# Optimization experiments

Hardware: AMD Instinct MI355X
Metric: run time of the kernel (lower is better)

Reference implementation:

```python
import jax, jax.numpy as jnp
import numpy as np

B, N = 16, 16384
K = 16        # num_keypoints
LATENT = 128
CAGE = 8
BN_EPS = 1e-5


def setup_inputs():
    key = jax.random.key(0)
    ks = jax.random.split(key, 40)
    def rn(i, shape, s=1.0):
        return jax.random.normal(ks[i], shape, dtype=jnp.float32) * s
    inp = {
        "source_points": rn(0, (B, N, 3)),
        "target_points": rn(1, (B, N, 3)),
        "enc_w1": rn(2, (64, 3), 0.3), "enc_b1": rn(3, (64,), 0.1),
        "bn1_gamma": 1.0 + rn(4, (64,), 0.1), "bn1_beta": rn(5, (64,), 0.1),
        "bn1_mean": rn(6, (64,), 0.1), "bn1_var": 0.5 + jax.random.uniform(ks[7], (64,), dtype=jnp.float32),
        "enc_w2": rn(8, (128, 64), 0.1), "enc_b2": rn(9, (128,), 0.1),
        "bn2_gamma": 1.0 + rn(10, (128,), 0.1), "bn2_beta": rn(11, (128,), 0.1),
        "bn2_mean": rn(12, (128,), 0.1), "bn2_var": 0.5 + jax.random.uniform(ks[13], (128,), dtype=jnp.float32),
        "enc_w3": rn(14, (LATENT, 128), 0.1), "enc_b3": rn(15, (LATENT,), 0.1),
        "bn3_gamma": 1.0 + rn(16, (LATENT,), 0.1), "bn3_beta": rn(17, (LATENT,), 0.1),
        "bn3_mean": rn(18, (LATENT,), 0.1), "bn3_var": 0.5 + jax.random.uniform(ks[19], (LATENT,), dtype=jnp.float32),
        "kp_w1": rn(20, (128, LATENT), 0.1), "kp_b1": rn(21, (128,), 0.1),
        "kp_w2": rn(22, (K * 3, 128), 0.1), "kp_b2": rn(23, (K * 3,), 0.1),
        "cg_w1": rn(24, (128, K * 3), 0.1), "cg_b1": rn(25, (128,), 0.1),
        "cg_w2": rn(26, (CAGE ** 3 * 3, 128), 0.05), "cg_b2": rn(27, (CAGE ** 3 * 3,), 0.01),
    }
    return inp


def _bn(x, g, b, m, v):
    # inference-mode BatchNorm1d over channel (last) dim
    return (x - m) * jax.lax.rsqrt(v + BN_EPS) * g + b


def _encode(pts, w1, b1, g1, be1, m1, v1, w2, b2, g2, be2, m2, v2, w3, b3, g3, be3, m3, v3):
    # pointwise 1x1 convs == per-point linear layers; pts: (B, N, 3)
    h = jax.nn.relu(_bn(jnp.einsum('bnc,oc->bno', pts, w1) + b1, g1, be1, m1, v1))
    h = jax.nn.relu(_bn(jnp.einsum('bnc,oc->bno', h, w2) + b2, g2, be2, m2, v2))
    h = jax.nn.relu(_bn(jnp.einsum('bnc,oc->bno', h, w3) + b3, g3, be3, m3, v3))
    return h.max(axis=1)  # global max-pool -> (B, LATENT)


def _fps_one(pts, kps):
    # pts: (N,3), kps: (K,3). Same math as the torch loop: iterative farthest-point
    # selection; recomputing cdist to selected[:i] each step == incremental min-dist.
    # squared distances preserve argmax/min of euclidean distances.
    d0 = jnp.sum((pts[:, None, :] - kps[None, :, :]) ** 2, -1).min(axis=1)
    sel0 = pts[jnp.argmax(d0)]
    mind = jnp.sum((pts - sel0) ** 2, -1)
    def step(mind, _):
        sel = pts[jnp.argmax(mind)]
        return jnp.minimum(mind, jnp.sum((pts - sel) ** 2, -1)), sel
    _, sels = jax.lax.scan(step, mind, None, length=K - 1)
    return jnp.concatenate([sel0[None], sels], axis=0)  # (K, 3)


def _fps(points, keypoints):
    return jax.vmap(_fps_one)(points, keypoints)


def _cage_deform(pts, disp):
    # pts: (B,N,3), disp: (B,C,C,C,3). Batched trilinear interpolation on the cage.
    C = CAGE
    lin = jnp.linspace(0.0, 1.0, C)
    grid = jnp.stack(jnp.meshgrid(lin, lin, lin, indexing='ij'), axis=-1)
    cage = grid[None] + disp
    cf = cage.reshape(cage.shape[0], C * C * C, 3)
    pmin = pts.min(axis=1, keepdims=True)
    pmax = pts.max(axis=1, keepdims=True)
    t = (pts - pmin) / (pmax - pmin + 1e-6) * (C - 1)
    idx = jnp.clip(t.astype(jnp.int32), 0, C - 2)   # trunc == floor (t >= 0)
    w = t - idx.astype(t.dtype)
    u, v, z = idx[..., 0], idx[..., 1], idx[..., 2]
    wx, wy, wz = w[..., 0:1], w[..., 1:2], w[..., 2:3]
    def corner(du, dv, dz):
        flat = (u + du) * C * C + (v + dv) * C + (z + dz)      # (B,N)
        flat = jnp.broadcast_to(flat[..., None], flat.shape + (3,))
        return jnp.take_along_axis(cf, flat, axis=1)            # (B,N,3)
    d = ((1 - wx) * (1 - wy) * (1 - wz) * corner(0, 0, 0)
         + wx * (1 - wy) * (1 - wz) * corner(1, 0, 0)
         + (1 - wx) * wy * (1 - wz) * corner(0, 1, 0)
         + wx * wy * (1 - wz) * corner(1, 1, 0)
         + (1 - wx) * (1 - wy) * wz * corner(0, 0, 1)
         + wx * (1 - wy) * wz * corner(1, 0, 1)
         + (1 - wx) * wy * wz * corner(0, 1, 1)
         + wx * wy * wz * corner(1, 1, 1))
    return pts + d


def reference(source_points, target_points, enc_w1, enc_b1, bn1_gamma, bn1_beta, bn1_mean, bn1_var, enc_w2, enc_b2, bn2_gamma, bn2_beta, bn2_mean, bn2_var, enc_w3, enc_b3, bn3_gamma, bn3_beta, bn3_mean, bn3_var, kp_w1, kp_b1, kp_w2, kp_b2, cg_w1, cg_b1, cg_w2, cg_b2):
    enc = lambda p: _encode(p, enc_w1, enc_b1, bn1_gamma, bn1_beta, bn1_mean, bn1_var,
                            enc_w2, enc_b2, bn2_gamma, bn2_beta, bn2_mean, bn2_var,
                            enc_w3, enc_b3, bn3_gamma, bn3_beta, bn3_mean, bn3_var)
    src_lat = enc(source_points)
    tgt_lat = enc(target_points)
    kp = lambda lat: (jax.nn.relu(lat @ kp_w1.T + kp_b1) @ kp_w2.T + kp_b2).reshape(-1, K, 3)
    src_kp = _fps(source_points, kp(src_lat))
    tgt_kp = _fps(target_points, kp(tgt_lat))
    diff = (tgt_kp - src_kp).reshape(-1, K * 3)
    disp = (jax.nn.relu(diff @ cg_w1.T + cg_b1) @ cg_w2.T + cg_b2).reshape(-1, CAGE, CAGE, CAGE, 3)
    deformed = _cage_deform(source_points, disp)
    return (deformed, src_kp, tgt_kp)
```

## Files before the change

kernel.cpp:

```cpp
#include <hip/hip_runtime.h>

#define B_ 16
#define N_ 16384
#define K_ 16

enum : int {
  WS_LAT  = 0,
  WS_SEL  = 5632,
  WS_PMIN = 7168,
  WS_PMAX = 7216,
  WS_CF   = 7264,
  WS_W1F  = 31840,
  WS_B1F  = 32032,
  WS_WB2H = 32096,
  WS_WB2L = 36192,
  WS_B2F  = 40288,
  WS_WB3H = 40416,
  WS_B3F  = 56800,
  WS_WB3L = 56928,
  WS_END  = 73312
};

enum : int { OUT_DEF=0, OUT_SRCKP=786432, OUT_TGTKP=787200 };

typedef _Float16 f16x8 __attribute__((ext_vector_type(8)));
typedef _Float16 f16x2 __attribute__((ext_vector_type(2)));
typedef float    f32x4 __attribute__((ext_vector_type(4)));

__device__ __forceinline__ float dist2rn(float px,float py,float pz,float sx,float sy,float sz){
  float dx=__fsub_rn(px,sx), dy=__fsub_rn(py,sy), dz=__fsub_rn(pz,sz);
  return __fadd_rn(__fadd_rn(__fmul_rn(dx,dx),__fmul_rn(dy,dy)),__fmul_rn(dz,dz));
}

struct EncW {
  const float *w1,*b1,*g1,*be1,*m1,*v1;
  const float *w2,*b2,*g2,*be2,*m2,*v2;
  const float *w3,*b3,*g3,*be3,*m3,*v3;
};

__device__ __forceinline__ float bn_scale(const float* g, const float* v, int ch){
  return g[ch] * (1.0f / sqrtf(v[ch] + 1e-5f));
}

__global__ void prep_kernel(EncW a, float* ws){
  const int stride = gridDim.x*blockDim.x;
  const int tid = blockIdx.x*blockDim.x + threadIdx.x;
  for (int i=tid;i<4096;i+=stride)
    ws[WS_LAT+i] = 0.0f;
  for (int i=tid;i<192;i+=stride){
    int o=i/3;
    ws[WS_W1F+i] = a.w1[i] * bn_scale(a.g1,a.v1,o);
  }
  for (int i=tid;i<64;i+=stride){
    float s = bn_scale(a.g1,a.v1,i);
    ws[WS_B1F+i] = (a.b1[i] - a.m1[i])*s + a.be1[i];
  }
  for (int i=tid;i<8192;i+=stride){
    int j = i & 7, frag = i >> 3;
    int l = frag & 63, nk = frag >> 6;
    int kt = nk & 1, nt = nk >> 1;
    int c = kt*32 + ((l>>4)<<3) + j;
    int o = nt*16 + (l&15);
    float v = a.w2[o*64+c] * bn_scale(a.g2,a.v2,o);
    _Float16 h = (_Float16)v;
    ((_Float16*)(ws+WS_WB2H))[i] = h;
    ((_Float16*)(ws+WS_WB2L))[i] = (_Float16)(v - (float)h);
  }
  for (int i=tid;i<128;i+=stride){
    float s = bn_scale(a.g2,a.v2,i);
    ws[WS_B2F+i] = (a.b2[i] - a.m2[i])*s + a.be2[i];
  }
  for (int i=tid;i<32768;i+=stride){
    int j = i & 7, frag = i >> 3;
    int l = frag & 63, nk = frag >> 6;
    int kt = nk & 3, nt = nk >> 2;
    int c = kt*32 + ((l>>4)<<3) + j;
    int o = nt*16 + (l&15);
    float v = a.w3[o*128+c] * bn_scale(a.g3,a.v3,o);
    _Float16 h = (_Float16)v;
    ((_Float16*)(ws+WS_WB3H))[i] = h;
    ((_Float16*)(ws+WS_WB3L))[i] = (_Float16)(v - (float)h);
  }
  for (int i=tid;i<128;i+=stride){
    float s = bn_scale(a.g3,a.v3,i);
    ws[WS_B3F+i] = (a.b3[i] - a.m3[i])*s + a.be3[i];
  }
}

__global__ __launch_bounds__(256, 4) void encode_kernel(const float* __restrict__ src,
                                                        const float* __restrict__ tgt,
                                                        const float* __restrict__ ws,
                                                        float* __restrict__ lat){
  const int cloud = blockIdx.y;
  const int tile  = blockIdx.x;
  const int t = threadIdx.x;
  const int lane = t & 63;
  const int wn = __builtin_amdgcn_readfirstlane(t >> 6);
  const int lr = lane & 15;
  const int lg = lane >> 4;

  __shared__ alignas(16) _Float16 A[16384];
  _Float16* AH1 = A;
  _Float16* AL1 = A + 4096;
  _Float16* AH2 = A;
  _Float16* AL2 = A + 8192;

  const float* base = ((cloud < B_) ? (src + (size_t)cloud*N_*3)
                                    : (tgt + (size_t)(cloud-B_)*N_*3))
                      + (size_t)tile*64*3;

  {
    const int pt = t >> 2, q = t & 3;
    const float x = base[pt*3+0], y = base[pt*3+1], z = base[pt*3+2];
    const float* w1 = ws + WS_W1F;
    const float* b1 = ws + WS_B1F;
    const int swz = (pt & 7) << 3;
    #pragma unroll
    for (int cc = 0; cc < 16; cc += 2){
      const int o = q*16 + cc;
      float v0 = fmaf(w1[o*3+2], z, fmaf(w1[o*3+1], y, w1[o*3+0]*x)) + b1[o];
      float v1 = fmaf(w1[o*3+5], z, fmaf(w1[o*3+4], y, w1[o*3+3]*x)) + b1[o+1];
      v0 = fmaxf(v0, 0.0f); v1 = fmaxf(v1, 0.0f);
      f16x2 h, l;
      h[0] = (_Float16)v0;              h[1] = (_Float16)v1;
      l[0] = (_Float16)(v0 - (float)h[0]); l[1] = (_Float16)(v1 - (float)h[1]);
      const int idx = (pt*64 + o) ^ swz;
      *(f16x2*)&AH1[idx] = h;
      *(f16x2*)&AL1[idx] = l;
    }
  }
  __syncthreads();

  f32x4 acc2[4][2];
  #pragma unroll
  for (int m=0;m<4;m++){
    #pragma unroll
    for (int n=0;n<2;n++) acc2[m][n] = (f32x4){0.f,0.f,0.f,0.f};
  }
  {
    const _Float16* wb2h = (const _Float16*)(ws + WS_WB2H);
    const _Float16* wb2l = (const _Float16*)(ws + WS_WB2L);
    const int swz = (lr & 7) << 3;
    #pragma unroll
    for (int kt=0; kt<2; kt++){
      f16x8 bh[2], bl[2];
      #pragma unroll
      for (int n=0;n<2;n++){
        const int fi = (((wn*2+n)*2 + kt)*64 + lane)*8;
        bh[n] = *(const f16x8*)(wb2h + fi);
        bl[n] = *(const f16x8*)(wb2l + fi);
      }
      #pragma unroll
      for (int m=0;m<4;m++){
        const int row = m*16 + lr;
        const int idx = (row*64 + kt*32 + lg*8) ^ swz;
        const f16x8 ah = *(const f16x8*)&AH1[idx];
        const f16x8 al = *(const f16x8*)&AL1[idx];
        #pragma unroll
        for (int n=0;n<2;n++){
          acc2[m][n] = __builtin_amdgcn_mfma_f32_16x16x32_f16(ah, bh[n], acc2[m][n], 0,0,0);
          acc2[m][n] = __builtin_amdgcn_mfma_f32_16x16x32_f16(ah, bl[n], acc2[m][n], 0,0,0);
          acc2[m][n] = __builtin_amdgcn_mfma_f32_16x16x32_f16(al, bh[n], acc2[m][n], 0,0,0);
        }
      }
    }
  }
  __syncthreads();

  {
    const float* b2 = ws + WS_B2F;
    #pragma unroll
    for (int n=0;n<2;n++){
      const int ch = wn*32 + n*16 + lr;
      const float b = b2[ch];
      #pragma unroll
      for (int m=0;m<4;m++){
        #pragma unroll
        for (int r=0;r<4;r++){
          const int row = m*16 + lg*4 + r;
          const float v = fmaxf(acc2[m][n][r] + b, 0.0f);
          const _Float16 hi = (_Float16)v;
          const _Float16 lo = (_Float16)(v - (float)hi);
          const int idx = (row*128 + ch) ^ ((row & 7) << 3);
          AH2[idx] = hi;
          AL2[idx] = lo;
        }
      }
    }
  }
  __syncthreads();

  f32x4 acc3[4][2];
  #pragma unroll
  for (int m=0;m<4;m++){
    #pragma unroll
    for (int n=0;n<2;n++) acc3[m][n] = (f32x4){0.f,0.f,0.f,0.f};
  }
  {
    const _Float16* wb3h = (const _Float16*)(ws + WS_WB3H);
    const _Float16* wb3l = (const _Float16*)(ws + WS_WB3L);
    const int swz = (lr & 7) << 3;
    #pragma unroll
    for (int kt=0; kt<4; kt++){
      f16x8 bh[2], bl[2];
      #pragma unroll
      for (int n=0;n<2;n++){
        const int fi = (((wn*2+n)*4 + kt)*64 + lane)*8;
        bh[n] = *(const f16x8*)(wb3h + fi);
        bl[n] = *(const f16x8*)(wb3l + fi);
      }
      #pragma unroll
      for (int m=0;m<4;m++){
        const int row = m*16 + lr;
        const int idx = (row*128 + kt*32 + lg*8) ^ swz;
        const f16x8 ah = *(const f16x8*)&AH2[idx];
        const f16x8 al = *(const f16x8*)&AL2[idx];
        #pragma unroll
        for (int n=0;n<2;n++){
          acc3[m][n] = __builtin_amdgcn_mfma_f32_16x16x32_f16(ah, bh[n], acc3[m][n], 0,0,0);
          acc3[m][n] = __builtin_amdgcn_mfma_f32_16x16x32_f16(ah, bl[n], acc3[m][n], 0,0,0);
          acc3[m][n] = __builtin_amdgcn_mfma_f32_16x16x32_f16(al, bh[n], acc3[m][n], 0,0,0);
        }
      }
    }
  }

  {
    const float* b3 = ws + WS_B3F;
    #pragma unroll
    for (int n=0;n<2;n++){
      const int ch = wn*32 + n*16 + lr;
      const float b = b3[ch];
      float x = 0.0f;
      #pragma unroll
      for (int m=0;m<4;m++){
        #pragma unroll
        for (int r=0;r<4;r++)
          x = fmaxf(x, acc3[m][n][r] + b);
      }
      x = fmaxf(x, __shfl_xor(x, 16, 64));
      x = fmaxf(x, __shfl_xor(x, 32, 64));
      if (lane < 16)
        atomicMax((unsigned*)(lat + cloud*128 + ch), __float_as_uint(x));
    }
  }
}

__device__ __forceinline__ void fps_round(int r, int t, int wv,
                                          float bv, int bi, float bx, float by, float bz,
                                          float (*cv)[16], int (*ci)[16],
                                          float (*cx)[16], float (*cy)[16], float (*cz)[16],
                                          float* ws, float* out, int cloud,
                                          float& s0, float& s1, float& s2){
  float v = bv; int i = bi;
  #pragma unroll
  for (int m=1;m<64;m<<=1){
    float v2=__shfl_xor(v,m,64); int i2=__shfl_xor(i,m,64);
    if (v2 > v || (v2 == v && i2 < i)){ v=v2; i=i2; }
  }
  const int p = r & 1;
  if ((i >> 4) == t){ cv[p][wv]=v; ci[p][wv]=i; cx[p][wv]=bx; cy[p][wv]=by; cz[p][wv]=bz; }
  __syncthreads();
  float wvv = cv[p][0]; int wi = ci[p][0]; int slot = 0;
  #pragma unroll
  for (int e=1;e<16;e++){
    float v2=cv[p][e]; int i2=ci[p][e];
    if (v2 > wvv || (v2 == wvv && i2 < wi)){ wvv=v2; wi=i2; slot=e; }
  }
  s0 = cx[p][slot]; s1 = cy[p][slot]; s2 = cz[p][slot];
  if (t == 0){
    float* sw = ws + WS_SEL + cloud*48 + r*3;
    sw[0]=s0; sw[1]=s1; sw[2]=s2;
    size_t o = (cloud<B_) ? (size_t)(OUT_SRCKP + cloud*48 + r*3)
                          : (size_t)(OUT_TGTKP + (cloud-B_)*48 + r*3);
    out[o]=s0; out[o+1]=s1; out[o+2]=s2;
  }
}

__global__ __launch_bounds__(1024, 4) void fps_kernel(const float* __restrict__ src,
                                                      const float* __restrict__ tgt,
                                                      const float* __restrict__ kw1,
                                                      const float* __restrict__ kb1,
                                                      const float* __restrict__ kw2,
                                                      const float* __restrict__ kb2,
                                                      float* ws, float* out){
  const int cloud = blockIdx.x; const int t = threadIdx.x;
  const int wv = t >> 6;
  const int lane = t & 63;
  const float* base = (cloud < B_) ? (src + (size_t)cloud*N_*3)
                                   : (tgt + (size_t)cloud*N_*3 - (size_t)B_*N_*3);
  __shared__ float kpl[48];
  __shared__ float h[128];
  __shared__ float cv[2][16]; __shared__ int ci[2][16];
  __shared__ float cx[2][16]; __shared__ float cy[2][16]; __shared__ float cz[2][16];
  __shared__ float red[96];

  float px[16], py[16], pz[16];
  {
    const float4* b4 = (const float4*)(base + (size_t)t*48);
    #pragma unroll
    for (int q=0;q<4;q++){
      float4 va=b4[q*3], vb=b4[q*3+1], vc=b4[q*3+2];
      px[q*4  ]=va.x; py[q*4  ]=va.y; pz[q*4  ]=va.z;
      px[q*4+1]=va.w; py[q*4+1]=vb.x; pz[q*4+1]=vb.y;
      px[q*4+2]=vb.z; py[q*4+2]=vb.w; pz[q*4+2]=vc.x;
      px[q*4+3]=vc.y; py[q*4+3]=vc.z; pz[q*4+3]=vc.w;
    }
  }

  if (cloud < B_){
    float mn0=3.4e38f,mn1=3.4e38f,mn2=3.4e38f, mx0=-3.4e38f,mx1=-3.4e38f,mx2=-3.4e38f;
    #pragma unroll
    for (int k=0;k<16;k++){
      mn0=fminf(mn0,px[k]); mn1=fminf(mn1,py[k]); mn2=fminf(mn2,pz[k]);
      mx0=fmaxf(mx0,px[k]); mx1=fmaxf(mx1,py[k]); mx2=fmaxf(mx2,pz[k]);
    }
    #pragma unroll
    for (int m=1;m<64;m<<=1){
      mn0=fminf(mn0,__shfl_xor(mn0,m,64)); mx0=fmaxf(mx0,__shfl_xor(mx0,m,64));
      mn1=fminf(mn1,__shfl_xor(mn1,m,64)); mx1=fmaxf(mx1,__shfl_xor(mx1,m,64));
      mn2=fminf(mn2,__shfl_xor(mn2,m,64)); mx2=fmaxf(mx2,__shfl_xor(mx2,m,64));
    }
    if (lane==0){
      red[wv*6+0]=mn0; red[wv*6+1]=mn1; red[wv*6+2]=mn2;
      red[wv*6+3]=mx0; red[wv*6+4]=mx1; red[wv*6+5]=mx2;
    }
    __syncthreads();
    if (t < 6){
      float v = red[t];
      for (int e=1;e<16;e++){
        float v2 = red[e*6+t];
        v = (t<3) ? fminf(v,v2) : fmaxf(v,v2);
      }
      if (t<3) ws[WS_PMIN + cloud*3 + t] = v;
      else     ws[WS_PMAX + cloud*3 + (t-3)] = v;
    }
  }
  __syncthreads();

  const float* lat = ws + WS_LAT + cloud*128;
  if (t < 128){
    float acc = kb1[t];
    const float* w = kw1 + t*128;
    for (int c=0;c<128;c++) acc = fmaf(lat[c], w[c], acc);
    h[t] = fmaxf(acc, 0.0f);
  }
  __syncthreads();
  if (t < 48){
    float acc = kb2[t];
    const float* w = kw2 + t*128;
    for (int c=0;c<128;c++) acc = fmaf(h[c], w[c], acc);
    kpl[t] = acc;
  }
  __syncthreads();

  float mind[16];
  #pragma unroll
  for (int k=0;k<16;k++) mind[k] = 3.4028235e38f;
  for (int j=0;j<K_;j++){
    const float sx=kpl[j*3], sy=kpl[j*3+1], sz=kpl[j*3+2];
    #pragma unroll
    for (int k=0;k<16;k++)
      mind[k] = fminf(mind[k], dist2rn(px[k],py[k],pz[k], sx,sy,sz));
  }

  float bv = -1.0f; int bi = 0; float bx=0.f, by=0.f, bz=0.f;
  #pragma unroll
  for (int k=0;k<16;k++){
    if (mind[k] > bv){ bv=mind[k]; bi=t*16+k; bx=px[k]; by=py[k]; bz=pz[k]; }
  }
  float s0, s1, s2;
  fps_round(0, t, wv, bv, bi, bx, by, bz, cv, ci, cx, cy, cz, ws, out, cloud, s0, s1, s2);

  bv = -1.0f; bi = 0;
  #pragma unroll
  for (int k=0;k<16;k++){
    float d = dist2rn(px[k],py[k],pz[k], s0,s1,s2);
    mind[k] = d;
    if (d > bv){ bv=d; bi=t*16+k; bx=px[k]; by=py[k]; bz=pz[k]; }
  }
  fps_round(1, t, wv, bv, bi, bx, by, bz, cv, ci, cx, cy, cz, ws, out, cloud, s0, s1, s2);

  for (int r=2; r<K_; ++r){
    bv = -1.0f; bi = 0;
    #pragma unroll
    for (int k=0;k<16;k++){
      float d = dist2rn(px[k],py[k],pz[k], s0,s1,s2);
      float m = fminf(mind[k], d);
      mind[k] = m;
      if (m > bv){ bv=m; bi=t*16+k; bx=px[k]; by=py[k]; bz=pz[k]; }
    }
    fps_round(r, t, wv, bv, bi, bx, by, bz, cv, ci, cx, cy, cz, ws, out, cloud, s0, s1, s2);
  }
}

__global__ void cage_mlp_kernel(const float* __restrict__ ws,
                                const float* __restrict__ cw1, const float* __restrict__ cb1,
                                const float* __restrict__ cw2, const float* __restrict__ cb2,
                                float* __restrict__ wsm){
  const int b = blockIdx.x >> 2, part = blockIdx.x & 3;
  const int t = threadIdx.x;
  __shared__ float diff[48]; __shared__ float h[128];
  if (t<48) diff[t] = __fsub_rn(ws[WS_SEL + (B_+b)*48 + t], ws[WS_SEL + b*48 + t]);
  __syncthreads();
  if (t<128){
    const float* w = cw1 + t*48;
    float acc = cb1[t];
    for (int j=0;j<48;j++) acc = fmaf(diff[j], w[j], acc);
    h[t] = fmaxf(acc, 0.0f);
  }
  __syncthreads();
  for (int o = part*384 + t; o < part*384 + 384; o += 256){
    const float* w = cw2 + o*128;
    float acc = cb2[o];
    for (int c=0;c<128;c++) acc = fmaf(h[c], w[c], acc);
    int flat = o/3, coord = o - flat*3;
    int u = flat>>6, v=(flat>>3)&7, z=flat&7;
    int g = (coord==0)?u:((coord==1)?v:z);
    float gv = (g==7)?1.0f:(float)g*(1.0f/7.0f);
    wsm[WS_CF + b*1536 + o] = gv + acc;
  }
}

__global__ __launch_bounds__(256) void deform_kernel(const float* __restrict__ src,
                                                     const float* __restrict__ ws,
                                                     float* __restrict__ out){
  const int b = blockIdx.y;
  const int n = blockIdx.x*256 + threadIdx.x;
  __shared__ float cf[1536];
  for (int i=threadIdx.x;i<1536;i+=256) cf[i] = ws[WS_CF + b*1536 + i];
  __syncthreads();

  const float* p = src + ((size_t)b*N_ + n)*3;
  float pt[3]; int id[3]; float w[3];
  #pragma unroll
  for (int c=0;c<3;c++){
    float pv = p[c];
    float mn  = ws[WS_PMIN+b*3+c];
    float mxv = ws[WS_PMAX+b*3+c];
    float denom = __fadd_rn(__fsub_rn(mxv, mn), 1e-6f);
    float tc = __fmul_rn(__fdiv_rn(__fsub_rn(pv, mn), denom), 7.0f);
    int ic = (int)tc; ic = min(max(ic,0),6);
    pt[c]=pv; id[c]=ic; w[c]=__fsub_rn(tc, (float)ic);
  }
  const int flat = (id[0]<<6) + (id[1]<<3) + id[2];
  const float* c000 = cf + flat*3;
  const float wx=w[0], wy=w[1], wz=w[2];
  const float ux=__fsub_rn(1.0f,wx), uy=__fsub_rn(1.0f,wy), uz=__fsub_rn(1.0f,wz);
  const float w000=__fmul_rn(__fmul_rn(ux,uy),uz);
  const float w100=__fmul_rn(__fmul_rn(wx,uy),uz);
  const float w010=__fmul_rn(__fmul_rn(ux,wy),uz);
  const float w110=__fmul_rn(__fmul_rn(wx,wy),uz);
  const float w001=__fmul_rn(__fmul_rn(ux,uy),wz);
  const float w101=__fmul_rn(__fmul_rn(wx,uy),wz);
  const float w011=__fmul_rn(__fmul_rn(ux,wy),wz);
  const float w111=__fmul_rn(__fmul_rn(wx,wy),wz);
  #pragma unroll
  for (int c=0;c<3;c++){
    float d = __fmul_rn(w000, c000[c]);
    d = __fadd_rn(d, __fmul_rn(w100, c000[192+c]));
    d = __fadd_rn(d, __fmul_rn(w010, c000[24+c]));
    d = __fadd_rn(d, __fmul_rn(w110, c000[216+c]));
    d = __fadd_rn(d, __fmul_rn(w001, c000[3+c]));
    d = __fadd_rn(d, __fmul_rn(w101, c000[195+c]));
    d = __fadd_rn(d, __fmul_rn(w011, c000[27+c]));
    d = __fadd_rn(d, __fmul_rn(w111, c000[219+c]));
    out[((size_t)b*N_+n)*3 + c] = __fadd_rn(pt[c], d);
  }
}

extern "C" void kernel_launch(void* const* d_in, const int* in_sizes, int n_in,
                              void* d_out, int out_size, void* d_ws, size_t ws_size,
                              hipStream_t stream){
  const float* src = (const float*)d_in[0];
  const float* tgt = (const float*)d_in[1];
  float* ws = (float*)d_ws;
  float* out = (float*)d_out;

  EncW ew;
  ew.w1 =(const float*)d_in[2];  ew.b1 =(const float*)d_in[3];
  ew.g1 =(const float*)d_in[4];  ew.be1=(const float*)d_in[5];
  ew.m1 =(const float*)d_in[6];  ew.v1 =(const float*)d_in[7];
  ew.w2 =(const float*)d_in[8];  ew.b2 =(const float*)d_in[9];
  ew.g2 =(const float*)d_in[10]; ew.be2=(const float*)d_in[11];
  ew.m2 =(const float*)d_in[12]; ew.v2 =(const float*)d_in[13];
  ew.w3 =(const float*)d_in[14]; ew.b3 =(const float*)d_in[15];
  ew.g3 =(const float*)d_in[16]; ew.be3=(const float*)d_in[17];
  ew.m3 =(const float*)d_in[18]; ew.v3 =(const float*)d_in[19];

  prep_kernel<<<128, 256, 0, stream>>>(ew, ws);
  encode_kernel<<<dim3(256,32), 256, 0, stream>>>(src, tgt, ws, ws + WS_LAT);
  fps_kernel<<<32, 1024, 0, stream>>>(src, tgt,
      (const float*)d_in[20], (const float*)d_in[21],
      (const float*)d_in[22], (const float*)d_in[23], ws, out);
  cage_mlp_kernel<<<64, 256, 0, stream>>>(ws,
      (const float*)d_in[24], (const float*)d_in[25],
      (const float*)d_in[26], (const float*)d_in[27], ws);
  deform_kernel<<<dim3(64,16), 256, 0, stream>>>(src, ws, out);
}
```

Before: 302.9 us.

## Fuse cage MLP into deform kernel and hoist encoder layer-2 weights

Drops the separate cage MLP launch by computing the cage coefficients inside each deform block, which now handles 1024 points with 4 points per thread. This removes one kernel launch and the workspace round trip, but every deform block redundantly computes the full 1536x128 cage MLP. The encoder loads its layer-2 MFMA weight fragments before layer 1 so they overlap with it, replaces index arithmetic with precomputed LDS byte pointers, and raises the launch-bounds occupancy hint from 4 to 5 blocks.

```diff
diff --git a/kernel.cpp b/kernel.cpp
--- a/kernel.cpp
+++ b/kernel.cpp
@@ -87,7 +87,7 @@
   }
 }
 
-__global__ __launch_bounds__(256, 4) void encode_kernel(const float* __restrict__ src,
+__global__ __launch_bounds__(256, 5) void encode_kernel(const float* __restrict__ src,
                                                         const float* __restrict__ tgt,
                                                         const float* __restrict__ ws,
                                                         float* __restrict__ lat){
@@ -100,21 +100,34 @@
   const int lg = lane >> 4;
 
   __shared__ alignas(16) _Float16 A[16384];
-  _Float16* AH1 = A;
-  _Float16* AL1 = A + 4096;
-  _Float16* AH2 = A;
-  _Float16* AL2 = A + 8192;
 
   const float* base = ((cloud < B_) ? (src + (size_t)cloud*N_*3)
                                     : (tgt + (size_t)(cloud-B_)*N_*3))
                       + (size_t)tile*64*3;
+
+  f16x8 b2h[2][2], b2l[2][2];
+  {
+    const _Float16* wb2h = (const _Float16*)(ws + WS_WB2H);
+    const _Float16* wb2l = (const _Float16*)(ws + WS_WB2L);
+    #pragma unroll
+    for (int kt=0; kt<2; kt++){
+      #pragma unroll
+      for (int n=0; n<2; n++){
+        const int fi = (((wn*2+n)*2 + kt)*64 + lane)*8;
+        b2h[kt][n] = *(const f16x8*)(wb2h + fi);
+        b2l[kt][n] = *(const f16x8*)(wb2l + fi);
+      }
+    }
+  }
 
   {
     const int pt = t >> 2, q = t & 3;
     const float x = base[pt*3+0], y = base[pt*3+1], z = base[pt*3+2];
     const float* w1 = ws + WS_W1F;
     const float* b1 = ws + WS_B1F;
-    const int swz = (pt & 7) << 3;
+    const int swz1 = (pt & 7) << 3;
+    _Float16* AH1 = A;
+    _Float16* AL1 = A + 4096;
     #pragma unroll
     for (int cc = 0; cc < 16; cc += 2){
       const int o = q*16 + cc;
@@ -124,13 +137,15 @@
       f16x2 h, l;
       h[0] = (_Float16)v0;              h[1] = (_Float16)v1;
       l[0] = (_Float16)(v0 - (float)h[0]); l[1] = (_Float16)(v1 - (float)h[1]);
-      const int idx = (pt*64 + o) ^ swz;
+      const int idx = (pt*64 + o) ^ swz1;
       *(f16x2*)&AH1[idx] = h;
       *(f16x2*)&AL1[idx] = l;
     }
   }
   __syncthreads();
 
+  const int swz = (lr & 7) << 3;
+
   f32x4 acc2[4][2];
   #pragma unroll
   for (int m=0;m<4;m++){
@@ -138,29 +153,20 @@
     for (int n=0;n<2;n++) acc2[m][n] = (f32x4){0.f,0.f,0.f,0.f};
   }
   {
-    const _Float16* wb2h = (const _Float16*)(ws + WS_WB2H);
-    const _Float16* wb2l = (const _Float16*)(ws + WS_WB2L);
-    const int swz = (lr & 7) << 3;
+    const char* pA0 = (const char*)A + lr*128 + ((( 0 + lg*8) ^ swz) << 1);
+    const char* pA1 = (const char*)A + lr*128 + (((32 + lg*8) ^ swz) << 1);
     #pragma unroll
     for (int kt=0; kt<2; kt++){
-      f16x8 bh[2], bl[2];
-      #pragma unroll
-      for (int n=0;n<2;n++){
-        const int fi = (((wn*2+n)*2 + kt)*64 + lane)*8;
-        bh[n] = *(const f16x8*)(wb2h + fi);
-        bl[n] = *(const f16x8*)(wb2l + fi);
-      }
+      const char* pA = kt ? pA1 : pA0;
       #pragma unroll
       for (int m=0;m<4;m++){
-        const int row = m*16 + lr;
-        const int idx = (row*64 + kt*32 + lg*8) ^ swz;
-        const f16x8 ah = *(const f16x8*)&AH1[idx];
-        const f16x8 al = *(const f16x8*)&AL1[idx];
+        const f16x8 ah = *(const f16x8*)(pA + m*2048);
+        const f16x8 al = *(const f16x8*)(pA + m*2048 + 8192);
         #pragma unroll
         for (int n=0;n<2;n++){
-          acc2[m][n] = __builtin_amdgcn_mfma_f32_16x16x32_f16(ah, bh[n], acc2[m][n], 0,0,0);
-          acc2[m][n] = __builtin_amdgcn_mfma_f32_16x16x32_f16(ah, bl[n], acc2[m][n], 0,0,0);
-          acc2[m][n] = __builtin_amdgcn_mfma_f32_16x16x32_f16(al, bh[n], acc2[m][n], 0,0,0);
+          acc2[m][n] = __builtin_amdgcn_mfma_f32_16x16x32_f16(ah, b2h[kt][n], acc2[m][n], 0,0,0);
+          acc2[m][n] = __builtin_amdgcn_mfma_f32_16x16x32_f16(ah, b2l[kt][n], acc2[m][n], 0,0,0);
+          acc2[m][n] = __builtin_amdgcn_mfma_f32_16x16x32_f16(al, b2h[kt][n], acc2[m][n], 0,0,0);
         }
       }
     }
@@ -168,22 +174,21 @@
   __syncthreads();
 
   {
-    const float* b2 = ws + WS_B2F;
     #pragma unroll
     for (int n=0;n<2;n++){
       const int ch = wn*32 + n*16 + lr;
-      const float b = b2[ch];
+      const float b = ws[WS_B2F + ch];
       #pragma unroll
-      for (int m=0;m<4;m++){
+      for (int r=0;r<4;r++){
+        const int mask = ((lg*4 + r) & 7) << 3;
+        char* pW = (char*)A + ((ch ^ mask) << 1) + lg*1024 + r*256;
         #pragma unroll
-        for (int r=0;r<4;r++){
-          const int row = m*16 + lg*4 + r;
+        for (int m=0;m<4;m++){
           const float v = fmaxf(acc2[m][n][r] + b, 0.0f);
           const _Float16 hi = (_Float16)v;
           const _Float16 lo = (_Float16)(v - (float)hi);
-          const int idx = (row*128 + ch) ^ ((row & 7) << 3);
-          AH2[idx] = hi;
-          AL2[idx] = lo;
+          *(_Float16*)(pW + m*4096) = hi;
+          *(_Float16*)(pW + m*4096 + 16384) = lo;
         }
       }
     }
@@ -199,7 +204,7 @@
   {
     const _Float16* wb3h = (const _Float16*)(ws + WS_WB3H);
     const _Float16* wb3l = (const _Float16*)(ws + WS_WB3L);
-    const int swz = (lr & 7) << 3;
+    const char* pR = (const char*)A + lr*256;
     #pragma unroll
     for (int kt=0; kt<4; kt++){
       f16x8 bh[2], bl[2];
@@ -209,12 +214,11 @@
         bh[n] = *(const f16x8*)(wb3h + fi);
         bl[n] = *(const f16x8*)(wb3l + fi);
       }
+      const int c3 = ((kt*32 + lg*8) ^ swz) << 1;
       #pragma unroll
       for (int m=0;m<4;m++){
-        const int row = m*16 + lr;
-        const int idx = (row*128 + kt*32 + lg*8) ^ swz;
-        const f16x8 ah = *(const f16x8*)&AH2[idx];
-        const f16x8 al = *(const f16x8*)&AL2[idx];
+        const f16x8 ah = *(const f16x8*)(pR + c3 + m*4096);
+        const f16x8 al = *(const f16x8*)(pR + c3 + m*4096 + 16384);
         #pragma unroll
         for (int n=0;n<2;n++){
           acc3[m][n] = __builtin_amdgcn_mfma_f32_16x16x32_f16(ah, bh[n], acc3[m][n], 0,0,0);
@@ -394,78 +398,82 @@
   }
 }
 
-__global__ void cage_mlp_kernel(const float* __restrict__ ws,
-                                const float* __restrict__ cw1, const float* __restrict__ cb1,
-                                const float* __restrict__ cw2, const float* __restrict__ cb2,
-                                float* __restrict__ wsm){
-  const int b = blockIdx.x >> 2, part = blockIdx.x & 3;
+__global__ __launch_bounds__(256) void deform_kernel(const float* __restrict__ src,
+                                                     const float* __restrict__ cw1,
+                                                     const float* __restrict__ cb1,
+                                                     const float* __restrict__ cw2,
+                                                     const float* __restrict__ cb2,
+                                                     const float* __restrict__ ws,
+                                                     float* __restrict__ out){
+  const int b = blockIdx.y;
   const int t = threadIdx.x;
-  __shared__ float diff[48]; __shared__ float h[128];
+  __shared__ float cf[1536];
+  __shared__ float diff[48];
+  __shared__ float hh[128];
+
   if (t<48) diff[t] = __fsub_rn(ws[WS_SEL + (B_+b)*48 + t], ws[WS_SEL + b*48 + t]);
   __syncthreads();
   if (t<128){
     const float* w = cw1 + t*48;
     float acc = cb1[t];
     for (int j=0;j<48;j++) acc = fmaf(diff[j], w[j], acc);
-    h[t] = fmaxf(acc, 0.0f);
-  }
-  __syncthreads();
-  for (int o = part*384 + t; o < part*384 + 384; o += 256){
+    hh[t] = fmaxf(acc, 0.0f);
+  }
+  __syncthreads();
+  for (int o = t; o < 1536; o += 256){
     const float* w = cw2 + o*128;
     float acc = cb2[o];
-    for (int c=0;c<128;c++) acc = fmaf(h[c], w[c], acc);
+    for (int c=0;c<128;c++) acc = fmaf(hh[c], w[c], acc);
     int flat = o/3, coord = o - flat*3;
     int u = flat>>6, v=(flat>>3)&7, z=flat&7;
     int g = (coord==0)?u:((coord==1)?v:z);
     float gv = (g==7)?1.0f:(float)g*(1.0f/7.0f);
-    wsm[WS_CF + b*1536 + o] = gv + acc;
-  }
-}
-
-__global__ __launch_bounds__(256) void deform_kernel(const float* __restrict__ src,
-                                                     const float* __restrict__ ws,
-                                                     float* __restrict__ out){
-  const int b = blockIdx.y;
-  const int n = blockIdx.x*256 + threadIdx.x;
-  __shared__ float cf[1536];
-  for (int i=threadIdx.x;i<1536;i+=256) cf[i] = ws[WS_CF + b*1536 + i];
-  __syncthreads();
-
-  const float* p = src + ((size_t)b*N_ + n)*3;
-  float pt[3]; int id[3]; float w[3];
-  #pragma unroll
-  for (int c=0;c<3;c++){
-    float pv = p[c];
-    float mn  = ws[WS_PMIN+b*3+c];
-    float mxv = ws[WS_PMAX+b*3+c];
-    float denom = __fadd_rn(__fsub_rn(mxv, mn), 1e-6f);
-    float tc = __fmul_rn(__fdiv_rn(__fsub_rn(pv, mn), denom), 7.0f);
-    int ic = (int)tc; ic = min(max(ic,0),6);
-    pt[c]=pv; id[c]=ic; w[c]=__fsub_rn(tc, (float)ic);
-  }
-  const int flat = (id[0]<<6) + (id[1]<<3) + id[2];
-  const float* c000 = cf + flat*3;
-  const float wx=w[0], wy=w[1], wz=w[2];
-  const float ux=__fsub_rn(1.0f,wx), uy=__fsub_rn(1.0f,wy), uz=__fsub_rn(1.0f,wz);
-  const float w000=__fmul_rn(__fmul_rn(ux,uy),uz);
-  const float w100=__fmul_rn(__fmul_rn(wx,uy),uz);
-  const float w010=__fmul_rn(__fmul_rn(ux,wy),uz);
-  const float w110=__fmul_rn(__fmul_rn(wx,wy),uz);
-  const float w001=__fmul_rn(__fmul_rn(ux,uy),wz);
-  const float w101=__fmul_rn(__fmul_rn(wx,uy),wz);
-  const float w011=__fmul_rn(__fmul_rn(ux,wy),wz);
-  const float w111=__fmul_rn(__fmul_rn(wx,wy),wz);
-  #pragma unroll
-  for (int c=0;c<3;c++){
-    float d = __fmul_rn(w000, c000[c]);
-    d = __fadd_rn(d, __fmul_rn(w100, c000[192+c]));
-    d = __fadd_rn(d, __fmul_rn(w010, c000[24+c]));
-    d = __fadd_rn(d, __fmul_rn(w110, c000[216+c]));
-    d = __fadd_rn(d, __fmul_rn(w001, c000[3+c]));
-    d = __fadd_rn(d, __fmul_rn(w101, c000[195+c]));
-    d = __fadd_rn(d, __fmul_rn(w011, c000[27+c]));
-    d = __fadd_rn(d, __fmul_rn(w111, c000[219+c]));
-    out[((size_t)b*N_+n)*3 + c] = __fadd_rn(pt[c], d);
+    cf[o] = gv + acc;
+  }
+  __syncthreads();
+
+  const float mn0 = ws[WS_PMIN+b*3+0], mn1 = ws[WS_PMIN+b*3+1], mn2 = ws[WS_PMIN+b*3+2];
+  const float mx0 = ws[WS_PMAX+b*3+0], mx1 = ws[WS_PMAX+b*3+1], mx2 = ws[WS_PMAX+b*3+2];
+
+  #pragma unroll
+  for (int k=0;k<4;k++){
+    const int n = blockIdx.x*1024 + k*256 + t;
+    const float* p = src + ((size_t)b*N_ + n)*3;
+    float pt[3]; int id[3]; float w[3];
+    #pragma unroll
+    for (int c=0;c<3;c++){
+      float pv = p[c];
+      float mnv = (c==0)?mn0:((c==1)?mn1:mn2);
+      float mxv = (c==0)?mx0:((c==1)?mx1:mx2);
+      float denom = __fadd_rn(__fsub_rn(mxv, mnv), 1e-6f);
+      float tc = __fmul_rn(__fdiv_rn(__fsub_rn(pv, mnv), denom), 7.0f);
+      int ic = (int)tc; ic = min(max(ic,0),6);
+      pt[c]=pv; id[c]=ic; w[c]=__fsub_rn(tc, (float)ic);
+    }
+    const int flat = (id[0]<<6) + (id[1]<<3) + id[2];
+    const float* c000 = cf + flat*3;
+    const float wx=w[0], wy=w[1], wz=w[2];
+    const float ux=__fsub_rn(1.0f,wx), uy=__fsub_rn(1.0f,wy), uz=__fsub_rn(1.0f,wz);
+    const float w000=__fmul_rn(__fmul_rn(ux,uy),uz);
+    const float w100=__fmul_rn(__fmul_rn(wx,uy),uz);
+    const float w010=__fmul_rn(__fmul_rn(ux,wy),uz);
+    const float w110=__fmul_rn(__fmul_rn(wx,wy),uz);
+    const float w001=__fmul_rn(__fmul_rn(ux,uy),wz);
+    const float w101=__fmul_rn(__fmul_rn(wx,uy),wz);
+    const float w011=__fmul_rn(__fmul_rn(ux,wy),wz);
+    const float w111=__fmul_rn(__fmul_rn(wx,wy),wz);
+    #pragma unroll
+    for (int c=0;c<3;c++){
+      float d = __fmul_rn(w000, c000[c]);
+      d = __fadd_rn(d, __fmul_rn(w100, c000[192+c]));
+      d = __fadd_rn(d, __fmul_rn(w010, c000[24+c]));
+      d = __fadd_rn(d, __fmul_rn(w110, c000[216+c]));
+      d = __fadd_rn(d, __fmul_rn(w001, c000[3+c]));
+      d = __fadd_rn(d, __fmul_rn(w101, c000[195+c]));
+      d = __fadd_rn(d, __fmul_rn(w011, c000[27+c]));
+      d = __fadd_rn(d, __fmul_rn(w111, c000[219+c]));
+      out[((size_t)b*N_+n)*3 + c] = __fadd_rn(pt[c], d);
+    }
   }
 }
 
@@ -482,8 +490,8 @@
   ew.g1 =(const float*)d_in[4];  ew.be1=(const float*)d_in[5];
   ew.m1 =(const float*)d_in[6];  ew.v1 =(const float*)d_in[7];
   ew.w2 =(const float*)d_in[8];  ew.b2 =(const float*)d_in[9];
+  ew.m2 =(const float*)d_in[12]; ew.v2 =(const float*)d_in[13];
   ew.g2 =(const float*)d_in[10]; ew.be2=(const float*)d_in[11];
-  ew.m2 =(const float*)d_in[12]; ew.v2 =(const float*)d_in[13];
   ew.w3 =(const float*)d_in[14]; ew.b3 =(const float*)d_in[15];
   ew.g3 =(const float*)d_in[16]; ew.be3=(const float*)d_in[17];
   ew.m3 =(const float*)d_in[18]; ew.v3 =(const float*)d_in[19];
@@ -493,8 +501,7 @@
   fps_kernel<<<32, 1024, 0, stream>>>(src, tgt,
       (const float*)d_in[20], (const float*)d_in[21],
       (const float*)d_in[22], (const float*)d_in[23], ws, out);
-  cage_mlp_kernel<<<64, 256, 0, stream>>>(ws,
+  deform_kernel<<<dim3(16,16), 256, 0, stream>>>(src,
       (const float*)d_in[24], (const float*)d_in[25],
-      (const float*)d_in[26], (const float*)d_in[27], ws);
-  deform_kernel<<<dim3(64,16), 256, 0, stream>>>(src, ws, out);
-}
+      (const float*)d_in[26], (const float*)d_in[27], ws, out);
+}
```

After: 298.4 us. About the same (-1.5%).
